# Performance work log

Hardware: AMD Instinct MI355X
Metric: run time of the kernel (lower is better)

Reference implementation:

```python
import jax, jax.numpy as jnp
import numpy as np

N_NODES = 50000
N_EDGES = 600000
N_GRAPHS = 1000
IN_DIM = 128   # atom_feat_dim
HID = 128      # emb_dim
NEG_SLOPE = 0.01


def setup_inputs() -> dict:
    key = jax.random.key(0)
    k = jax.random.split(key, 6)
    drug_x = jax.random.normal(k[0], (N_NODES, IN_DIM), dtype=jnp.float32)
    edge_index = jax.random.randint(k[1], (2, N_EDGES), 0, N_NODES, dtype=jnp.int32)
    batch = jnp.sort(jax.random.randint(k[2], (N_NODES,), 0, N_GRAPHS, dtype=jnp.int32))
    # GCNConv parameters (glorot-ish init for weights, zero bias, as in PyG)
    W1 = jax.random.normal(k[3], (IN_DIM, HID), dtype=jnp.float32) * (1.0 / np.sqrt(IN_DIM))
    b1 = jnp.zeros((HID,), dtype=jnp.float32)
    W2 = jax.random.normal(k[4], (HID, HID), dtype=jnp.float32) * (1.0 / np.sqrt(HID))
    b2 = jnp.zeros((HID,), dtype=jnp.float32)
    return {"drug_x": drug_x, "W1": W1, "b1": b1, "W2": W2, "b2": b2,
            "edge_index": edge_index, "batch": batch}


def _gcn_conv(x, W, b, src, dst, n_nodes):
    """PyG GCNConv: lin -> add self-loops -> deg^-1/2 sym norm -> scatter-add -> +bias."""
    h = x @ W  # [N, H]
    ones = jnp.ones(src.shape[0], dtype=h.dtype)
    # degree on the target side, +1 for the self-loop
    deg = jax.ops.segment_sum(ones, dst, num_segments=n_nodes) + 1.0
    dinv = jax.lax.rsqrt(deg)  # [N]
    coef = dinv[src] * dinv[dst]  # [E]
    agg = jax.ops.segment_sum(h[src] * coef[:, None], dst, num_segments=n_nodes)
    # self-loop contribution: dinv[i]*dinv[i]*h[i]
    agg = agg + h * (dinv * dinv)[:, None]
    return agg + b


def _leaky_relu(x):
    return jnp.where(x > 0, x, NEG_SLOPE * x)


def reference(drug_x, W1, b1, W2, b2, edge_index, batch):
    src, dst = edge_index[0], edge_index[1]
    n = drug_x.shape[0]
    h = _leaky_relu(_gcn_conv(drug_x, W1, b1, src, dst, n))  # dropout = identity (eval)
    h = _leaky_relu(_gcn_conv(h, W2, b2, src, dst, n))
    # global_mean_pool over graph ids
    sums = jax.ops.segment_sum(h, batch, num_segments=N_GRAPHS)
    counts = jax.ops.segment_sum(jnp.ones((n,), h.dtype), batch, num_segments=N_GRAPHS)
    return sums / jnp.maximum(counts, 1.0)[:, None]
```

## Files before the change

kernel.cpp:

```cpp
#include <hip/hip_runtime.h>

#define DIM 128
#define NEG_SLOPE 0.01f
#define ELLW 64
#define CPAD 16
#define LDA 136
#define SPLIT 4
#define WPAD 132

typedef short short8 __attribute__((ext_vector_type(8)));
typedef float f32x4 __attribute__((ext_vector_type(4)));

__device__ __forceinline__ unsigned short f2bf(float f) {
    unsigned u = __float_as_uint(f);
    u = u + 0x7FFFu + ((u >> 16) & 1u);
    return (unsigned short)(u >> 16);
}
__device__ __forceinline__ float bf2f(unsigned short s) {
    return __uint_as_float((unsigned)s << 16);
}

__global__ __launch_bounds__(256) void k_fillprep(const int* __restrict__ src,
                                                  const int* __restrict__ dst,
                                                  const int* __restrict__ batch,
                                                  int* __restrict__ cursorPad,
                                                  unsigned short* __restrict__ eSrcU,
                                                  const float* __restrict__ W1,
                                                  const float* __restrict__ W2,
                                                  unsigned short* __restrict__ Wt1,
                                                  unsigned short* __restrict__ Wt2,
                                                  int* __restrict__ gOff,
                                                  int nE, int nN, int nG) {
    int i = blockIdx.x * 256 + threadIdx.x;
    if (i < nE) {
        int s = src[i], d = dst[i];
        int pos = atomicAdd(&cursorPad[d * CPAD], 1);
        if (pos < ELLW) eSrcU[(size_t)d * ELLW + pos] = (unsigned short)s;
    }
    if (i < nN) {
        int b1 = batch[i];
        int b0 = (i == 0) ? -1 : batch[i - 1];
        for (int g = b0 + 1; g <= b1; ++g) gOff[g] = i;
        if (i == nN - 1) {
            for (int g = b1 + 1; g <= nG; ++g) gOff[g] = nN;
        }
    }
    if (i < 32768) {
        const float* W = (i < 16384) ? W1 : W2;
        unsigned short* Wt = (i < 16384) ? Wt1 : Wt2;
        int j = i & 16383;
        int k = j >> 7, n = j & 127;
        Wt[n * 128 + k] = f2bf(W[k * 128 + n]);
    }
}

#define ACCUM(v)                                         \
    do {                                                 \
        acc[0] += bf2f((v).x & 0xFFFFu);                 \
        acc[1] += __uint_as_float((v).x & 0xFFFF0000u);  \
        acc[2] += bf2f((v).y & 0xFFFFu);                 \
        acc[3] += __uint_as_float((v).y & 0xFFFF0000u);  \
        acc[4] += bf2f((v).z & 0xFFFFu);                 \
        acc[5] += __uint_as_float((v).z & 0xFFFF0000u);  \
        acc[6] += bf2f((v).w & 0xFFFFu);                 \
        acc[7] += __uint_as_float((v).w & 0xFFFF0000u);  \
    } while (0)

#define ACCUMF(v, s)                                                      \
    do {                                                                  \
        acc[0] = fmaf(bf2f((v).x & 0xFFFFu), (s), acc[0]);                \
        acc[1] = fmaf(__uint_as_float((v).x & 0xFFFF0000u), (s), acc[1]); \
        acc[2] = fmaf(bf2f((v).y & 0xFFFFu), (s), acc[2]);                \
        acc[3] = fmaf(__uint_as_float((v).y & 0xFFFF0000u), (s), acc[3]); \
        acc[4] = fmaf(bf2f((v).z & 0xFFFFu), (s), acc[4]);                \
        acc[5] = fmaf(__uint_as_float((v).z & 0xFFFF0000u), (s), acc[5]); \
        acc[6] = fmaf(bf2f((v).w & 0xFFFFu), (s), acc[6]);                \
        acc[7] = fmaf(__uint_as_float((v).w & 0xFFFF0000u), (s), acc[7]); \
    } while (0)

#define U16AT(e, j) ((int)((j & 1) ? (((j >> 1) == 0 ? (e).x : (j >> 1) == 1 ? (e).y : (j >> 1) == 2 ? (e).z : (e).w) >> 16) \
                                   : (((j >> 1) == 0 ? (e).x : (j >> 1) == 1 ? (e).y : (j >> 1) == 2 ? (e).z : (e).w) & 0xFFFFu)))

__device__ __forceinline__ void gather_body(const uint4* __restrict__ h4,
                                            const int* __restrict__ cursorPad,
                                            const unsigned short* __restrict__ eSrcU,
                                            const float* __restrict__ bias,
                                            int i, int l, float* acc) {
    const int cnt = cursorPad[i * CPAD];
    const uint4 e0 = *(const uint4*)&eSrcU[(size_t)i * ELLW];
    const uint4 e1 = *(const uint4*)&eSrcU[(size_t)i * ELLW + 8];
    const uint4 hv = h4[(size_t)i * 16 + l];

    const int deg = min(cnt, ELLW);
    const float di = rsqrtf((float)cnt + 1.0f);
    const unsigned un = 50000u;

    uint4 v[16];
#pragma unroll
    for (int j = 0; j < 8; ++j) {
        unsigned s = (unsigned)U16AT(e0, j);
        s = (s < un) ? s : 0u;
        v[j] = h4[(size_t)s * 16 + l];
    }
#pragma unroll
    for (int j = 0; j < 8; ++j) {
        unsigned s = (unsigned)U16AT(e1, j);
        s = (s < un) ? s : 0u;
        v[8 + j] = h4[(size_t)s * 16 + l];
    }

    acc[0] = bf2f(hv.x & 0xFFFFu);
    acc[1] = __uint_as_float(hv.x & 0xFFFF0000u);
    acc[2] = bf2f(hv.y & 0xFFFFu);
    acc[3] = __uint_as_float(hv.y & 0xFFFF0000u);
    acc[4] = bf2f(hv.z & 0xFFFFu);
    acc[5] = __uint_as_float(hv.z & 0xFFFF0000u);
    acc[6] = bf2f(hv.w & 0xFFFFu);
    acc[7] = __uint_as_float(hv.w & 0xFFFF0000u);

#pragma unroll
    for (int j = 0; j < 16; ++j) {
        float sc = (j < deg) ? 1.0f : 0.0f;
        ACCUMF(v[j], sc);
    }

    if (deg > 16) {
        const uint4 e2 = *(const uint4*)&eSrcU[(size_t)i * ELLW + 16];
        const uint4 e3 = *(const uint4*)&eSrcU[(size_t)i * ELLW + 24];
#pragma unroll
        for (int j = 0; j < 8; ++j) {
            unsigned s = (unsigned)U16AT(e2, j);
            s = (s < un) ? s : 0u;
            v[j] = h4[(size_t)s * 16 + l];
        }
#pragma unroll
        for (int j = 0; j < 8; ++j) {
            unsigned s = (unsigned)U16AT(e3, j);
            s = (s < un) ? s : 0u;
            v[8 + j] = h4[(size_t)s * 16 + l];
        }
#pragma unroll
        for (int j = 0; j < 16; ++j) {
            float sc = (16 + j < deg) ? 1.0f : 0.0f;
            ACCUMF(v[j], sc);
        }
        for (int e = 32; e < deg; ++e) {
            int s = (int)eSrcU[(size_t)i * ELLW + e];
            uint4 w0 = h4[(size_t)s * 16 + l];
            ACCUM(w0);
        }
    }

    float4 b0 = *(const float4*)&bias[l * 8];
    float4 b1 = *(const float4*)&bias[l * 8 + 4];
    acc[0] = acc[0] * di + b0.x; acc[0] = acc[0] > 0.f ? acc[0] : NEG_SLOPE * acc[0];
    acc[1] = acc[1] * di + b0.y; acc[1] = acc[1] > 0.f ? acc[1] : NEG_SLOPE * acc[1];
    acc[2] = acc[2] * di + b0.z; acc[2] = acc[2] > 0.f ? acc[2] : NEG_SLOPE * acc[2];
    acc[3] = acc[3] * di + b0.w; acc[3] = acc[3] > 0.f ? acc[3] : NEG_SLOPE * acc[3];
    acc[4] = acc[4] * di + b1.x; acc[4] = acc[4] > 0.f ? acc[4] : NEG_SLOPE * acc[4];
    acc[5] = acc[5] * di + b1.y; acc[5] = acc[5] > 0.f ? acc[5] : NEG_SLOPE * acc[5];
    acc[6] = acc[6] * di + b1.z; acc[6] = acc[6] > 0.f ? acc[6] : NEG_SLOPE * acc[6];
    acc[7] = acc[7] * di + b1.w; acc[7] = acc[7] > 0.f ? acc[7] : NEG_SLOPE * acc[7];
}

__global__ __launch_bounds__(256) void k_gemm1(const float* __restrict__ X,
                                               const unsigned short* __restrict__ Wt,
                                               const int* __restrict__ cursorPad,
                                               uint4* __restrict__ Y4, int nRows) {
    __shared__ unsigned short sA[64 * LDA];
    const int t = threadIdx.x;
    const int row0 = blockIdx.x * 64;

#pragma unroll
    for (int rep = 0; rep < 8; ++rep) {
        int idx = t + rep * 256;
        int r = idx >> 5, k4 = (idx & 31) * 4;
        int gr = row0 + r;
        float4 v = make_float4(0.f, 0.f, 0.f, 0.f);
        if (gr < nRows) v = *(const float4*)&X[(size_t)gr * 128 + k4];
        ushort4 p;
        p.x = f2bf(v.x); p.y = f2bf(v.y); p.z = f2bf(v.z); p.w = f2bf(v.w);
        *(ushort4*)&sA[r * LDA + k4] = p;
    }
    __syncthreads();

    const int wave = t >> 6, lane = t & 63;
    const int l15 = lane & 15;
    const int koff = (lane >> 4) * 8;
    const int arow = wave * 16 + l15;

    short8 a[4];
#pragma unroll
    for (int ks = 0; ks < 4; ++ks)
        a[ks] = *(const short8*)&sA[arow * LDA + ks * 32 + koff];

    f32x4 acc[8];
#pragma unroll
    for (int c = 0; c < 8; ++c) acc[c] = (f32x4){0.f, 0.f, 0.f, 0.f};
#pragma unroll
    for (int c = 0; c < 8; ++c) {
        const unsigned short* wp = Wt + (size_t)(c * 16 + l15) * 128 + koff;
#pragma unroll
        for (int ks = 0; ks < 4; ++ks) {
            short8 b = *(const short8*)(wp + ks * 32);
            acc[c] = __builtin_amdgcn_mfma_f32_16x16x32_bf16(a[ks], b, acc[c], 0, 0, 0);
        }
    }

    __syncthreads();
#pragma unroll
    for (int r = 0; r < 4; ++r) {
        int lrow = wave * 16 + (lane >> 4) * 4 + r;
        int gr = row0 + lrow;
        float dv = (gr < nRows) ? rsqrtf((float)cursorPad[gr * CPAD] + 1.0f) : 0.f;
#pragma unroll
        for (int c = 0; c < 8; ++c)
            sA[lrow * LDA + c * 16 + l15] = f2bf(acc[c][r] * dv);
    }
    __syncthreads();
#pragma unroll
    for (int p = 0; p < 4; ++p) {
        int idx = t + p * 256;
        int row = idx >> 4, chunk = idx & 15;
        int gr = row0 + row;
        if (gr < nRows)
            Y4[(size_t)gr * 16 + chunk] = *(const uint4*)&sA[row * LDA + chunk * 8];
    }
}

__global__ __launch_bounds__(256) void k_agg1(const uint4* __restrict__ h4,
                                              const int* __restrict__ cursorPad,
                                              const unsigned short* __restrict__ eSrcU,
                                              const float* __restrict__ bias,
                                              uint4* __restrict__ aggOut, int nN) {
    const int t = threadIdx.x;
    const int i = blockIdx.x * 16 + (t >> 4);
    const int l = t & 15;
    if (i >= nN) return;

    float acc[8];
    gather_body(h4, cursorPad, eSrcU, bias, i, l, acc);

    uint4 p;
    p.x = (unsigned)f2bf(acc[0]) | ((unsigned)f2bf(acc[1]) << 16);
    p.y = (unsigned)f2bf(acc[2]) | ((unsigned)f2bf(acc[3]) << 16);
    p.z = (unsigned)f2bf(acc[4]) | ((unsigned)f2bf(acc[5]) << 16);
    p.w = (unsigned)f2bf(acc[6]) | ((unsigned)f2bf(acc[7]) << 16);
    aggOut[(size_t)i * 16 + l] = p;
}

__global__ __launch_bounds__(256) void k_gemm2(const uint4* __restrict__ agg4,
                                               const unsigned short* __restrict__ Wt,
                                               const int* __restrict__ cursorPad,
                                               uint4* __restrict__ Y4, int nRows) {
    __shared__ unsigned short sA[64 * LDA];
    const int t = threadIdx.x;
    const int row0 = blockIdx.x * 64;

#pragma unroll
    for (int p = 0; p < 4; ++p) {
        int idx = t + p * 256;
        int row = idx >> 4, chunk = idx & 15;
        int gr = row0 + row;
        uint4 v = (uint4){0u, 0u, 0u, 0u};
        if (gr < nRows) v = agg4[(size_t)gr * 16 + chunk];
        *(uint4*)&sA[row * LDA + chunk * 8] = v;
    }
    __syncthreads();

    const int wave = t >> 6, lane = t & 63;
    const int l15 = lane & 15;
    const int koff = (lane >> 4) * 8;
    const int arow = wave * 16 + l15;

    short8 a[4];
#pragma unroll
    for (int ks = 0; ks < 4; ++ks)
        a[ks] = *(const short8*)&sA[arow * LDA + ks * 32 + koff];

    f32x4 acc[8];
#pragma unroll
    for (int c = 0; c < 8; ++c) acc[c] = (f32x4){0.f, 0.f, 0.f, 0.f};
#pragma unroll
    for (int c = 0; c < 8; ++c) {
        const unsigned short* wp = Wt + (size_t)(c * 16 + l15) * 128 + koff;
#pragma unroll
        for (int ks = 0; ks < 4; ++ks) {
            short8 b = *(const short8*)(wp + ks * 32);
            acc[c] = __builtin_amdgcn_mfma_f32_16x16x32_bf16(a[ks], b, acc[c], 0, 0, 0);
        }
    }

    __syncthreads();
#pragma unroll
    for (int r = 0; r < 4; ++r) {
        int lrow = wave * 16 + (lane >> 4) * 4 + r;
        int gr = row0 + lrow;
        float dv = (gr < nRows) ? rsqrtf((float)cursorPad[gr * CPAD] + 1.0f) : 0.f;
#pragma unroll
        for (int c = 0; c < 8; ++c)
            sA[lrow * LDA + c * 16 + l15] = f2bf(acc[c][r] * dv);
    }
    __syncthreads();
#pragma unroll
    for (int p = 0; p < 4; ++p) {
        int idx = t + p * 256;
        int row = idx >> 4, chunk = idx & 15;
        int gr = row0 + row;
        if (gr < nRows)
            Y4[(size_t)gr * 16 + chunk] = *(const uint4*)&sA[row * LDA + chunk * 8];
    }
}

__global__ __launch_bounds__(256, 4) void k_gp(const uint4* __restrict__ h4in,
                                               const int* __restrict__ cursorPad,
                                               const unsigned short* __restrict__ eSrcU,
                                               const float* __restrict__ bias,
                                               const int* __restrict__ gOff,
                                               float* __restrict__ out, int nN, int nG) {
    __shared__ float accW[4 * WPAD];
    const int g = blockIdx.x / SPLIT;
    const int part = blockIdx.x % SPLIT;
    const int t = threadIdx.x;
    const int beg = gOff[g], end = gOff[g + 1];
    const int lg = t >> 4, l = t & 15;
    const int wave = t >> 6, lane = t & 63;

    float acc8[8];
#pragma unroll
    for (int j = 0; j < 8; ++j) acc8[j] = 0.0f;

    for (int base = beg + part * 16; base < end; base += SPLIT * 16) {
        int i = base + lg;
        if (i < end) {
            float a[8];
            gather_body(h4in, cursorPad, eSrcU, bias, i, l, a);
#pragma unroll
            for (int j = 0; j < 8; ++j) acc8[j] += a[j];
        }
    }
#pragma unroll
    for (int j = 0; j < 8; ++j) {
        acc8[j] += __shfl_down(acc8[j], 32);
        acc8[j] += __shfl_down(acc8[j], 16);
    }
    if (lane < 16) {
        *(float4*)&accW[wave * WPAD + lane * 8] =
            make_float4(acc8[0], acc8[1], acc8[2], acc8[3]);
        *(float4*)&accW[wave * WPAD + lane * 8 + 4] =
            make_float4(acc8[4], acc8[5], acc8[6], acc8[7]);
    }
    __syncthreads();
    if (t < 128) {
        float s = accW[0 * WPAD + t] + accW[1 * WPAD + t] +
                  accW[2 * WPAD + t] + accW[3 * WPAD + t];
        float cnt = (float)(end - beg);
        atomicAdd(&out[(size_t)g * DIM + t], s / fmaxf(cnt, 1.0f));
    }
}

extern "C" void kernel_launch(void* const* d_in, const int* in_sizes, int n_in,
                              void* d_out, int out_size, void* d_ws, size_t ws_size,
                              hipStream_t stream) {
    const float* X  = (const float*)d_in[0];
    const float* W1 = (const float*)d_in[1];
    const float* b1 = (const float*)d_in[2];
    const float* W2 = (const float*)d_in[3];
    const float* b2 = (const float*)d_in[4];
    const int*   ei = (const int*)d_in[5];
    const int*   batch = (const int*)d_in[6];
    float* out = (float*)d_out;

    const int NN = in_sizes[0] / DIM;
    const int NE = in_sizes[5] / 2;
    const int NG = out_size / DIM;

    const int* src = ei;
    const int* dst = ei + NE;

    char* ws = (char*)d_ws;
    size_t o = 0;
    auto alloc = [&](size_t bytes) {
        char* p = ws + o;
        o += (bytes + 1023) & ~(size_t)1023;
        return p;
    };
    int* cursorPad = (int*)alloc((size_t)NN * CPAD * 4);
    int* gOff      = (int*)alloc((size_t)(NG + 1) * 4);
    unsigned short* Wt1 = (unsigned short*)alloc((size_t)16384 * 2);
    unsigned short* Wt2 = (unsigned short*)alloc((size_t)16384 * 2);
    unsigned short* eSrcU = (unsigned short*)alloc((size_t)NN * ELLW * 2);
    unsigned short* bufA = (unsigned short*)alloc((size_t)NN * DIM * 2);
    unsigned short* agg  = (unsigned short*)alloc((size_t)NN * DIM * 2);
    unsigned short* bufB = (unsigned short*)alloc((size_t)NN * DIM * 2);

    hipMemsetAsync(cursorPad, 0, (size_t)NN * CPAD * 4, stream);
    hipMemsetAsync(out, 0, (size_t)out_size * 4, stream);

    const int B = 256;

    k_fillprep<<<(NE + B - 1) / B, B, 0, stream>>>(src, dst, batch, cursorPad, eSrcU,
                                                   W1, W2, Wt1, Wt2, gOff, NE, NN, NG);

    k_gemm1<<<(NN + 63) / 64, B, 0, stream>>>(X, Wt1, cursorPad, (uint4*)bufA, NN);

    k_agg1<<<(NN + 15) / 16, B, 0, stream>>>((const uint4*)bufA, cursorPad, eSrcU,
                                             b1, (uint4*)agg, NN);

    k_gemm2<<<(NN + 63) / 64, B, 0, stream>>>((const uint4*)agg, Wt2, cursorPad,
                                              (uint4*)bufB, NN);

    k_gp<<<NG * SPLIT, B, 0, stream>>>((const uint4*)bufB, cursorPad, eSrcU, b2,
                                       gOff, out, NN, NG);
}
```

Before: 207.1 us.

## Split node features into column-chunked layout for cache-local edge gathers

Stores the intermediate bf16 node features as four 32-column chunks, each a contiguous [N,32] array, and assigns each aggregation/pool block to a single chunk. The random neighbour gathers for a given block then touch only a 3.2MB slice, which is meant to fit in L2/LLC and raise hit rates. Degree counts are compacted into a dense cntA array written by gemm1, edge-index loads become nontemporal, and the pooling kernel writes its output directly instead of zeroing it and using atomics. In exchange, edge lists are re-read four times (once per chunk) and each lane does a smaller 16-byte gather, so there is more index traffic.

```diff
diff --git a/kernel.cpp b/kernel.cpp
--- a/kernel.cpp
+++ b/kernel.cpp
@@ -5,11 +5,11 @@
 #define ELLW 64
 #define CPAD 16
 #define LDA 136
-#define SPLIT 4
-#define WPAD 132
+#define NCH 4
 
 typedef short short8 __attribute__((ext_vector_type(8)));
 typedef float f32x4 __attribute__((ext_vector_type(4)));
+typedef unsigned int ux4 __attribute__((ext_vector_type(4)));
 
 __device__ __forceinline__ unsigned short f2bf(float f) {
     unsigned u = __float_as_uint(f);
@@ -81,15 +81,15 @@
 #define U16AT(e, j) ((int)((j & 1) ? (((j >> 1) == 0 ? (e).x : (j >> 1) == 1 ? (e).y : (j >> 1) == 2 ? (e).z : (e).w) >> 16) \
                                    : (((j >> 1) == 0 ? (e).x : (j >> 1) == 1 ? (e).y : (j >> 1) == 2 ? (e).z : (e).w) & 0xFFFFu)))
 
-__device__ __forceinline__ void gather_body(const uint4* __restrict__ h4,
-                                            const int* __restrict__ cursorPad,
-                                            const unsigned short* __restrict__ eSrcU,
-                                            const float* __restrict__ bias,
-                                            int i, int l, float* acc) {
-    const int cnt = cursorPad[i * CPAD];
-    const uint4 e0 = *(const uint4*)&eSrcU[(size_t)i * ELLW];
-    const uint4 e1 = *(const uint4*)&eSrcU[(size_t)i * ELLW + 8];
-    const uint4 hv = h4[(size_t)i * 16 + l];
+__device__ __forceinline__ void gather_chunk(const uint4* __restrict__ hc,
+                                             const int* __restrict__ cntA,
+                                             const unsigned short* __restrict__ eSrcU,
+                                             const float* __restrict__ bias,
+                                             int i, int l, float* acc) {
+    const int cnt = cntA[i];
+    const ux4 e0 = __builtin_nontemporal_load((const ux4*)&eSrcU[(size_t)i * ELLW]);
+    const ux4 e1 = __builtin_nontemporal_load((const ux4*)&eSrcU[(size_t)i * ELLW + 8]);
+    const uint4 hv = hc[(size_t)i * 4 + l];
 
     const int deg = min(cnt, ELLW);
     const float di = rsqrtf((float)cnt + 1.0f);
@@ -100,13 +100,13 @@
     for (int j = 0; j < 8; ++j) {
         unsigned s = (unsigned)U16AT(e0, j);
         s = (s < un) ? s : 0u;
-        v[j] = h4[(size_t)s * 16 + l];
+        v[j] = hc[(size_t)s * 4 + l];
     }
 #pragma unroll
     for (int j = 0; j < 8; ++j) {
         unsigned s = (unsigned)U16AT(e1, j);
         s = (s < un) ? s : 0u;
-        v[8 + j] = h4[(size_t)s * 16 + l];
+        v[8 + j] = hc[(size_t)s * 4 + l];
     }
 
     acc[0] = bf2f(hv.x & 0xFFFFu);
@@ -125,19 +125,19 @@
     }
 
     if (deg > 16) {
-        const uint4 e2 = *(const uint4*)&eSrcU[(size_t)i * ELLW + 16];
-        const uint4 e3 = *(const uint4*)&eSrcU[(size_t)i * ELLW + 24];
+        const ux4 e2 = __builtin_nontemporal_load((const ux4*)&eSrcU[(size_t)i * ELLW + 16]);
+        const ux4 e3 = __builtin_nontemporal_load((const ux4*)&eSrcU[(size_t)i * ELLW + 24]);
 #pragma unroll
         for (int j = 0; j < 8; ++j) {
             unsigned s = (unsigned)U16AT(e2, j);
             s = (s < un) ? s : 0u;
-            v[j] = h4[(size_t)s * 16 + l];
+            v[j] = hc[(size_t)s * 4 + l];
         }
 #pragma unroll
         for (int j = 0; j < 8; ++j) {
             unsigned s = (unsigned)U16AT(e3, j);
             s = (s < un) ? s : 0u;
-            v[8 + j] = h4[(size_t)s * 16 + l];
+            v[8 + j] = hc[(size_t)s * 4 + l];
         }
 #pragma unroll
         for (int j = 0; j < 16; ++j) {
@@ -146,7 +146,7 @@
         }
         for (int e = 32; e < deg; ++e) {
             int s = (int)eSrcU[(size_t)i * ELLW + e];
-            uint4 w0 = h4[(size_t)s * 16 + l];
+            uint4 w0 = hc[(size_t)s * 4 + l];
             ACCUM(w0);
         }
     }
@@ -166,7 +166,8 @@
 __global__ __launch_bounds__(256) void k_gemm1(const float* __restrict__ X,
                                                const unsigned short* __restrict__ Wt,
                                                const int* __restrict__ cursorPad,
-                                               uint4* __restrict__ Y4, int nRows) {
+                                               uint4* __restrict__ Yc,
+                                               int* __restrict__ cntA, int nRows) {
     __shared__ unsigned short sA[64 * LDA];
     const int t = threadIdx.x;
     const int row0 = blockIdx.x * 64;
@@ -212,7 +213,9 @@
     for (int r = 0; r < 4; ++r) {
         int lrow = wave * 16 + (lane >> 4) * 4 + r;
         int gr = row0 + lrow;
-        float dv = (gr < nRows) ? rsqrtf((float)cursorPad[gr * CPAD] + 1.0f) : 0.f;
+        int cnt = (gr < nRows) ? cursorPad[gr * CPAD] : 0;
+        float dv = rsqrtf((float)cnt + 1.0f);
+        if (l15 == 0 && gr < nRows) cntA[gr] = cnt;
 #pragma unroll
         for (int c = 0; c < 8; ++c)
             sA[lrow * LDA + c * 16 + l15] = f2bf(acc[c][r] * dv);
@@ -221,38 +224,42 @@
 #pragma unroll
     for (int p = 0; p < 4; ++p) {
         int idx = t + p * 256;
-        int row = idx >> 4, chunk = idx & 15;
+        int row = idx >> 4, seg = idx & 15;
+        int c = seg >> 2, q = seg & 3;
         int gr = row0 + row;
         if (gr < nRows)
-            Y4[(size_t)gr * 16 + chunk] = *(const uint4*)&sA[row * LDA + chunk * 8];
-    }
-}
-
-__global__ __launch_bounds__(256) void k_agg1(const uint4* __restrict__ h4,
-                                              const int* __restrict__ cursorPad,
-                                              const unsigned short* __restrict__ eSrcU,
-                                              const float* __restrict__ bias,
-                                              uint4* __restrict__ aggOut, int nN) {
+            Yc[((size_t)c * nRows + gr) * 4 + q] = *(const uint4*)&sA[row * LDA + seg * 8];
+    }
+}
+
+__global__ __launch_bounds__(256) void k_agg1c(const uint4* __restrict__ hC,
+                                               const int* __restrict__ cntA,
+                                               const unsigned short* __restrict__ eSrcU,
+                                               const float* __restrict__ bias,
+                                               uint4* __restrict__ aggC, int nN) {
+    const int c = blockIdx.x & 3;
+    const int tile = blockIdx.x >> 2;
     const int t = threadIdx.x;
-    const int i = blockIdx.x * 16 + (t >> 4);
-    const int l = t & 15;
+    const int i = tile * 64 + (t >> 2);
+    const int l = t & 3;
     if (i >= nN) return;
 
+    const uint4* hc = hC + (size_t)c * nN * 4;
     float acc[8];
-    gather_body(h4, cursorPad, eSrcU, bias, i, l, acc);
+    gather_chunk(hc, cntA, eSrcU, bias + c * 32, i, l, acc);
 
     uint4 p;
     p.x = (unsigned)f2bf(acc[0]) | ((unsigned)f2bf(acc[1]) << 16);
     p.y = (unsigned)f2bf(acc[2]) | ((unsigned)f2bf(acc[3]) << 16);
     p.z = (unsigned)f2bf(acc[4]) | ((unsigned)f2bf(acc[5]) << 16);
     p.w = (unsigned)f2bf(acc[6]) | ((unsigned)f2bf(acc[7]) << 16);
-    aggOut[(size_t)i * 16 + l] = p;
-}
-
-__global__ __launch_bounds__(256) void k_gemm2(const uint4* __restrict__ agg4,
+    aggC[((size_t)c * nN + i) * 4 + l] = p;
+}
+
+__global__ __launch_bounds__(256) void k_gemm2(const uint4* __restrict__ aggC,
                                                const unsigned short* __restrict__ Wt,
-                                               const int* __restrict__ cursorPad,
-                                               uint4* __restrict__ Y4, int nRows) {
+                                               const int* __restrict__ cntA,
+                                               uint4* __restrict__ Yc, int nRows) {
     __shared__ unsigned short sA[64 * LDA];
     const int t = threadIdx.x;
     const int row0 = blockIdx.x * 64;
@@ -260,11 +267,12 @@
 #pragma unroll
     for (int p = 0; p < 4; ++p) {
         int idx = t + p * 256;
-        int row = idx >> 4, chunk = idx & 15;
+        int row = idx >> 4, seg = idx & 15;
+        int c = seg >> 2, q = seg & 3;
         int gr = row0 + row;
         uint4 v = (uint4){0u, 0u, 0u, 0u};
-        if (gr < nRows) v = agg4[(size_t)gr * 16 + chunk];
-        *(uint4*)&sA[row * LDA + chunk * 8] = v;
+        if (gr < nRows) v = aggC[((size_t)c * nRows + gr) * 4 + q];
+        *(uint4*)&sA[row * LDA + seg * 8] = v;
     }
     __syncthreads();
 
@@ -296,7 +304,7 @@
     for (int r = 0; r < 4; ++r) {
         int lrow = wave * 16 + (lane >> 4) * 4 + r;
         int gr = row0 + lrow;
-        float dv = (gr < nRows) ? rsqrtf((float)cursorPad[gr * CPAD] + 1.0f) : 0.f;
+        float dv = (gr < nRows) ? rsqrtf((float)cntA[gr] + 1.0f) : 0.f;
 #pragma unroll
         for (int c = 0; c < 8; ++c)
             sA[lrow * LDA + c * 16 + l15] = f2bf(acc[c][r] * dv);
@@ -305,36 +313,39 @@
 #pragma unroll
     for (int p = 0; p < 4; ++p) {
         int idx = t + p * 256;
-        int row = idx >> 4, chunk = idx & 15;
+        int row = idx >> 4, seg = idx & 15;
+        int c = seg >> 2, q = seg & 3;
         int gr = row0 + row;
         if (gr < nRows)
-            Y4[(size_t)gr * 16 + chunk] = *(const uint4*)&sA[row * LDA + chunk * 8];
-    }
-}
-
-__global__ __launch_bounds__(256, 4) void k_gp(const uint4* __restrict__ h4in,
-                                               const int* __restrict__ cursorPad,
-                                               const unsigned short* __restrict__ eSrcU,
-                                               const float* __restrict__ bias,
-                                               const int* __restrict__ gOff,
-                                               float* __restrict__ out, int nN, int nG) {
-    __shared__ float accW[4 * WPAD];
-    const int g = blockIdx.x / SPLIT;
-    const int part = blockIdx.x % SPLIT;
+            Yc[((size_t)c * nRows + gr) * 4 + q] = *(const uint4*)&sA[row * LDA + seg * 8];
+    }
+}
+
+__global__ __launch_bounds__(256) void k_gpc(const uint4* __restrict__ hC,
+                                             const int* __restrict__ cntA,
+                                             const unsigned short* __restrict__ eSrcU,
+                                             const float* __restrict__ bias,
+                                             const int* __restrict__ gOff,
+                                             float* __restrict__ out, int nN) {
+    __shared__ float accW[4 * 36];
+    const int c = blockIdx.x & 3;
+    const int g = blockIdx.x >> 2;
     const int t = threadIdx.x;
     const int beg = gOff[g], end = gOff[g + 1];
-    const int lg = t >> 4, l = t & 15;
+    const int l = t & 3;
     const int wave = t >> 6, lane = t & 63;
 
+    const uint4* hc = hC + (size_t)c * nN * 4;
+
     float acc8[8];
 #pragma unroll
     for (int j = 0; j < 8; ++j) acc8[j] = 0.0f;
 
-    for (int base = beg + part * 16; base < end; base += SPLIT * 16) {
-        int i = base + lg;
+    for (int base = beg; base < end; base += 64) {
+        int i = base + (t >> 2);
         if (i < end) {
             float a[8];
-            gather_body(h4in, cursorPad, eSrcU, bias, i, l, a);
+            gather_chunk(hc, cntA, eSrcU, bias + c * 32, i, l, a);
 #pragma unroll
             for (int j = 0; j < 8; ++j) acc8[j] += a[j];
         }
@@ -343,19 +354,18 @@
     for (int j = 0; j < 8; ++j) {
         acc8[j] += __shfl_down(acc8[j], 32);
         acc8[j] += __shfl_down(acc8[j], 16);
-    }
-    if (lane < 16) {
-        *(float4*)&accW[wave * WPAD + lane * 8] =
-            make_float4(acc8[0], acc8[1], acc8[2], acc8[3]);
-        *(float4*)&accW[wave * WPAD + lane * 8 + 4] =
-            make_float4(acc8[4], acc8[5], acc8[6], acc8[7]);
-    }
-    __syncthreads();
-    if (t < 128) {
-        float s = accW[0 * WPAD + t] + accW[1 * WPAD + t] +
-                  accW[2 * WPAD + t] + accW[3 * WPAD + t];
+        acc8[j] += __shfl_down(acc8[j], 8);
+        acc8[j] += __shfl_down(acc8[j], 4);
+    }
+    if (lane < 4) {
+#pragma unroll
+        for (int j = 0; j < 8; ++j) accW[wave * 36 + lane * 8 + j] = acc8[j];
+    }
+    __syncthreads();
+    if (t < 32) {
+        float s = accW[0 * 36 + t] + accW[1 * 36 + t] + accW[2 * 36 + t] + accW[3 * 36 + t];
         float cnt = (float)(end - beg);
-        atomicAdd(&out[(size_t)g * DIM + t], s / fmaxf(cnt, 1.0f));
+        out[(size_t)g * DIM + c * 32 + t] = s / fmaxf(cnt, 1.0f);
     }
 }
 
@@ -390,26 +400,26 @@
     unsigned short* Wt1 = (unsigned short*)alloc((size_t)16384 * 2);
     unsigned short* Wt2 = (unsigned short*)alloc((size_t)16384 * 2);
     unsigned short* eSrcU = (unsigned short*)alloc((size_t)NN * ELLW * 2);
+    int* cntA = (int*)alloc((size_t)NN * 4);
     unsigned short* bufA = (unsigned short*)alloc((size_t)NN * DIM * 2);
     unsigned short* agg  = (unsigned short*)alloc((size_t)NN * DIM * 2);
     unsigned short* bufB = (unsigned short*)alloc((size_t)NN * DIM * 2);
 
     hipMemsetAsync(cursorPad, 0, (size_t)NN * CPAD * 4, stream);
-    hipMemsetAsync(out, 0, (size_t)out_size * 4, stream);
 
     const int B = 256;
+    const int nT64 = (NN + 63) / 64;
 
     k_fillprep<<<(NE + B - 1) / B, B, 0, stream>>>(src, dst, batch, cursorPad, eSrcU,
                                                    W1, W2, Wt1, Wt2, gOff, NE, NN, NG);
 
-    k_gemm1<<<(NN + 63) / 64, B, 0, stream>>>(X, Wt1, cursorPad, (uint4*)bufA, NN);
-
-    k_agg1<<<(NN + 15) / 16, B, 0, stream>>>((const uint4*)bufA, cursorPad, eSrcU,
-                                             b1, (uint4*)agg, NN);
-
-    k_gemm2<<<(NN + 63) / 64, B, 0, stream>>>((const uint4*)agg, Wt2, cursorPad,
-                                              (uint4*)bufB, NN);
-
-    k_gp<<<NG * SPLIT, B, 0, stream>>>((const uint4*)bufB, cursorPad, eSrcU, b2,
-                                       gOff, out, NN, NG);
-}
+    k_gemm1<<<nT64, B, 0, stream>>>(X, Wt1, cursorPad, (uint4*)bufA, cntA, NN);
+
+    k_agg1c<<<nT64 * NCH, B, 0, stream>>>((const uint4*)bufA, cntA, eSrcU, b1,
+                                          (uint4*)agg, NN);
+
+    k_gemm2<<<nT64, B, 0, stream>>>((const uint4*)agg, Wt2, cntA, (uint4*)bufB, NN);
+
+    k_gpc<<<NG * NCH, B, 0, stream>>>((const uint4*)bufB, cntA, eSrcU, b2,
+                                      gOff, out, NN);
+}
```

New measurement: 213.1 us. 2.9% more time.
